# Performance work log

Hardware: AMD Instinct MI355X
Metric: run time of the kernel (lower is better)

## Reference

```python
import jax, jax.numpy as jnp
import numpy as np

L, N, E, D, H = 3, 20000, 320000, 128, 4
EPS = 1.1920929e-07  # torch RMSNorm default eps = finfo(float32).eps
NEG_SLOPE = 0.2      # PyG GATConv leaky_relu negative_slope


def rmsnorm(x, w):
    return x * jax.lax.rsqrt(jnp.mean(x * x, axis=-1, keepdims=True) + EPS) * w


def setup_inputs() -> dict:
    key = jax.random.key(0)
    ks = jax.random.split(key, 13)
    s = 0.02
    x = jax.random.normal(ks[0], (N, D), jnp.float32)
    src = jax.random.randint(ks[1], (E,), 0, N, dtype=jnp.int64)
    dst = jax.random.randint(ks[2], (E,), 0, N, dtype=jnp.int64)
    dst = jnp.where(dst == src, (dst + 1) % N, dst)  # no pre-existing self loops
    edge_index = jnp.stack([src, dst])
    return {
        "x": x,
        "W_gat": jax.random.normal(ks[3], (L, D, H * D), jnp.float32) * s,
        "att_src": jax.random.normal(ks[4], (L, H, D), jnp.float32) * s,
        "att_dst": jax.random.normal(ks[5], (L, H, D), jnp.float32) * s,
        "bias_gat": jax.random.normal(ks[6], (L, D), jnp.float32) * s,
        "W1": jax.random.normal(ks[7], (L, D, D), jnp.float32) * s,
        "b1": jax.random.normal(ks[8], (L, D), jnp.float32) * s,
        "W2": jax.random.normal(ks[9], (L, D, D), jnp.float32) * s,
        "b2": jax.random.normal(ks[10], (L, D), jnp.float32) * s,
        "norm1_w": jnp.ones((L, D), jnp.float32),
        "norm2_w": jnp.ones((L, D), jnp.float32),
        "edge_index": edge_index,
    }


def reference(x, W_gat, att_src, att_dst, bias_gat, W1, b1, W2, b2, norm1_w, norm2_w, edge_index):
    # PyG GATConv adds self loops by default
    loops = jnp.arange(N, dtype=edge_index.dtype)
    src = jnp.concatenate([edge_index[0], loops])  # [E+N]
    dst = jnp.concatenate([edge_index[1], loops])
    for i in range(L):
        # --- GATConv(hidden, hidden, heads=H, concat=False), dropout=0 (eval) ---
        xp = (x @ W_gat[i]).reshape(N, H, D)               # [N,H,D]
        a_s = jnp.einsum('nhd,hd->nh', xp, att_src[i])     # [N,H]
        a_d = jnp.einsum('nhd,hd->nh', xp, att_dst[i])
        e = jax.nn.leaky_relu(a_s[src] + a_d[dst], NEG_SLOPE)  # [E+N,H]
        m = jax.ops.segment_max(e, dst, num_segments=N)
        ex = jnp.exp(e - m[dst])
        denom = jax.ops.segment_sum(ex, dst, num_segments=N)
        alpha = ex / denom[dst]                             # segment softmax over incoming edges
        agg = jax.ops.segment_sum(alpha[:, :, None] * xp[src], dst, num_segments=N)  # [N,H,D]
        x_att = agg.mean(axis=1) + bias_gat[i]              # concat=False -> head mean, then bias
        # --- residual + RMSNorm ---
        x = rmsnorm(x + x_att, norm1_w[i])
        # --- FFN ---
        h = jax.nn.relu(x @ W1[i] + b1[i])
        h = h @ W2[i] + b2[i]
        x = rmsnorm(x + h, norm2_w[i])
    return x
```

## Files before the change

### kernel.cpp

```cpp
#include <hip/hip_runtime.h>
#include <hip/hip_bf16.h>

#define N_NODES 20000
#define NEDGE   320000
#define DIM     128
#define NH      4
#define HD      512
#define LAYERS  3
#define EPS_RMS 1.1920929e-07f
#define SLOPE   0.2f
#define NTILES  (N_NODES >> 4)

typedef __bf16 bf16_t;
typedef __bf16 bf16v2 __attribute__((ext_vector_type(2)));
typedef __bf16 bf16v8 __attribute__((ext_vector_type(8)));
typedef float  f32v4  __attribute__((ext_vector_type(4)));
typedef float  f32v2  __attribute__((ext_vector_type(2)));

__device__ __forceinline__ int clamp_node(int s) {
    return ((unsigned)s >= (unsigned)N_NODES) ? 0 : s;
}
__device__ __forceinline__ float leaky(float e) { return e > 0.f ? e : SLOPE * e; }
__device__ __forceinline__ unsigned char enc_fp8(float v) {
    int p = __builtin_amdgcn_cvt_pk_fp8_f32(v, v, 0, false);
    return (unsigned char)(p & 0xff);
}
__device__ __forceinline__ unsigned short enc_fp8_pair(float a, float b) {
    int p = __builtin_amdgcn_cvt_pk_fp8_f32(a, b, 0, false);
    return (unsigned short)(p & 0xffff);
}

__device__ __forceinline__ bool wave_detect_bf16(const unsigned short* xh) {
    int lane = threadIdx.x & 63;
    unsigned short hw = xh[2 * lane];
    int e = (hw >> 7) & 0xff;
    unsigned long long b = __ballot(e >= 96 && e <= 140);
    return __popcll(b) >= 48;
}
__device__ __forceinline__ bool wave_detect_i64(const int* ei) {
    int lane = threadIdx.x & 63;
    unsigned long long b = __ballot(ei[2 * lane + 1] != 0);
    return b == 0ULL;
}
__device__ __forceinline__ float raw_elem(const void* in, size_t j, bool isbf) {
    return isbf ? (float)((const bf16_t*)in)[j] : ((const float*)in)[j];
}
__device__ __forceinline__ bf16_t cvt_elem(const void* in, size_t j, bool isbf) {
    return isbf ? ((const bf16_t*)in)[j] : (bf16_t)((const float*)in)[j];
}
__device__ __forceinline__ int edge_src(const int* ei, int e, bool is64) {
    return clamp_node(is64 ? ei[2 * e] : ei[e]);
}
__device__ __forceinline__ int edge_dst(const int* ei, int e, bool is64) {
    return clamp_node(is64 ? ei[2 * NEDGE + 2 * e] : ei[NEDGE + e]);
}

__global__ __launch_bounds__(256) void prep_v(const void* x, const void* Wg,
                                              const void* aS, const void* aD,
                                              float* __restrict__ vS, float* __restrict__ vD,
                                              int* __restrict__ deg) {
    int gid = blockIdx.x * 256 + threadIdx.x;
    for (int i = gid; i < N_NODES; i += gridDim.x * 256) deg[i] = 0;
    bool isbf = wave_detect_bf16((const unsigned short*)x);
    int w = gid >> 6;
    if (w >= LAYERS * DIM * NH * 2) return;
    int lane = threadIdx.x & 63;
    int sd = w & 1, h = (w >> 1) & 3, k = (w >> 3) & 127, l = w >> 10;
    const void* att = sd ? aD : aS;
    size_t wbase = (size_t)l * DIM * HD + (size_t)k * HD + h * DIM;
    size_t abase = (size_t)l * NH * DIM + (size_t)h * DIM;
    int c = 2 * lane;
    float p = raw_elem(Wg, wbase + c, isbf) * raw_elem(att, abase + c, isbf)
            + raw_elem(Wg, wbase + c + 1, isbf) * raw_elem(att, abase + c + 1, isbf);
#pragma unroll
    for (int msk = 1; msk < 64; msk <<= 1) p += __shfl_xor(p, msk);
    if (lane == 0) {
        float* dst = sd ? vD : vS;
        dst[l * HD + h * DIM + k] = p;
    }
}

__global__ __launch_bounds__(256) void mega_setup(
        const void* x, const void* Wg, const void* W1, const void* W2,
        const void* bg, const void* b1, const void* b2, const void* n1, const void* n2,
        bf16_t* xb, bf16_t* WmixP, bf16_t* W1P, bf16_t* W2P,
        bf16_t* bgc, bf16_t* b1c, bf16_t* b2c, bf16_t* n1c, bf16_t* n2c,
        const int* ei, int* deg,
        const float* vS, const float* vD,
        float* a_s, float* a_d, unsigned short* x8,
        int convBlocks, int histBlocks) {
    const int NX  = N_NODES * DIM;
    const int NWG = LAYERS * DIM * HD;
    const int NW1 = LAYERS * DIM * DIM;
    const int NV  = LAYERS * DIM;
    int b = (int)blockIdx.x;
    if (b >= convBlocks + histBlocks) {
        bool isbf = wave_detect_bf16((const unsigned short*)x);
        int lane = threadIdx.x & 63;
        int n = (b - convBlocks - histBlocks) * 4 + (int)(threadIdx.x >> 6);
        if (n >= N_NODES) return;
        int c = 2 * lane;
        float f0 = raw_elem(x, (size_t)n * DIM + c, isbf);
        float f1 = raw_elem(x, (size_t)n * DIM + c + 1, isbf);
        x8[n * 64 + lane] = enc_fp8_pair(f0, f1);
#pragma unroll
        for (int h = 0; h < NH; ++h) {
            float ps = f0 * vS[h * DIM + c] + f1 * vS[h * DIM + c + 1];
            float pd = f0 * vD[h * DIM + c] + f1 * vD[h * DIM + c + 1];
#pragma unroll
            for (int msk = 1; msk < 64; msk <<= 1) {
                ps += __shfl_xor(ps, msk);
                pd += __shfl_xor(pd, msk);
            }
            if (lane == 0) {
                a_s[n * 4 + h] = ps;
                a_d[n * 4 + h] = pd;
            }
        }
        return;
    }
    if (b >= convBlocks) {
        bool is64 = wave_detect_i64(ei);
        int e = (b - convBlocks) * 256 + threadIdx.x;
        if (e < NEDGE) atomicAdd(&deg[edge_dst(ei, e, is64)], 1);
        return;
    }
    bool isbf = wave_detect_bf16((const unsigned short*)x);
    int i = b * 256 + threadIdx.x;
    if (i < NX) { xb[i] = cvt_elem(x, i, isbf); return; }
    i -= NX;
    if (i < NWG) {
        int l = i >> 16;
        int r = i & 65535;
        int j = r & 7;
        int lane2 = (r >> 3) & 63;
        int mm = lane2 & 15, kqq = lane2 >> 4;
        int tt = (r >> 9) & 1;
        int kk = (r >> 10) & 15;
        int wvv = r >> 14;
        int kidx = kk * 32 + kqq * 8 + j;
        int h = kidx >> 7, kp = kidx & 127;
        int c = 32 * wvv + tt * 16 + mm;
        WmixP[i] = cvt_elem(Wg, (size_t)l * DIM * HD + (size_t)kp * HD + h * DIM + c, isbf);
        return;
    }
    i -= NWG;
    if (i < NW1) {
        int l = i / 16384;
        int r = i & 16383;
        int j = r & 7;
        int lane2 = (r >> 3) & 63;
        int mm = lane2 & 15, kqq = lane2 >> 4;
        int tt = (r >> 9) & 1;
        int ks = (r >> 10) & 3;
        int wvv = r >> 12;
        int k = ks * 32 + kqq * 8 + j;
        int c = 32 * wvv + tt * 16 + mm;
        W1P[i] = cvt_elem(W1, (size_t)l * DIM * DIM + (size_t)k * DIM + c, isbf);
        return;
    }
    i -= NW1;
    if (i < NW1) {
        int l = i / 16384;
        int r = i & 16383;
        int j = r & 7;
        int lane2 = (r >> 3) & 63;
        int mm = lane2 & 15, kqq = lane2 >> 4;
        int tt = (r >> 9) & 1;
        int ks = (r >> 10) & 3;
        int wvv = r >> 12;
        int k = ks * 32 + kqq * 8 + j;
        int c = 32 * wvv + tt * 16 + mm;
        W2P[i] = cvt_elem(W2, (size_t)l * DIM * DIM + (size_t)k * DIM + c, isbf);
        return;
    }
    i -= NW1;
    if (i >= 5 * NV) return;
    int seg = i / NV, k = i - seg * NV;
    if (seg == 0) bgc[k] = cvt_elem(bg, k, isbf);
    else if (seg == 1) b1c[k] = cvt_elem(b1, k, isbf);
    else if (seg == 2) b2c[k] = cvt_elem(b2, k, isbf);
    else if (seg == 3) n1c[k] = cvt_elem(n1, k, isbf);
    else n2c[k] = cvt_elem(n2, k, isbf);
}

__global__ __launch_bounds__(1024) void scan_kernel(const int* __restrict__ deg,
                                                    int* __restrict__ row_ptr,
                                                    int* __restrict__ cursor) {
    __shared__ int wsum[16];
    int tid = threadIdx.x, lane = tid & 63, wv = tid >> 6;
    int v[20];
    int base = tid * 20;
    int tot = 0;
    if (base < N_NODES) {
        const int4* d4 = reinterpret_cast<const int4*>(deg + base);
#pragma unroll
        for (int j = 0; j < 5; ++j) {
            int4 q = d4[j];
            v[4 * j]     = q.x;
            v[4 * j + 1] = q.y;
            v[4 * j + 2] = q.z;
            v[4 * j + 3] = q.w;
        }
#pragma unroll
        for (int i = 0; i < 20; ++i) tot += v[i];
    }
    int x = tot;
#pragma unroll
    for (int off = 1; off < 64; off <<= 1) {
        int t = __shfl_up(x, off);
        if (lane >= off) x += t;
    }
    if (lane == 63) wsum[wv] = x;
    __syncthreads();
    if (wv == 0) {
        int s = (lane < 16) ? wsum[lane] : 0;
#pragma unroll
        for (int off = 1; off < 16; off <<= 1) {
            int t = __shfl_up(s, off);
            if (lane >= off) s += t;
        }
        if (lane < 16) wsum[lane] = s;
    }
    __syncthreads();
    int off0 = ((wv == 0) ? 0 : wsum[wv - 1]) + (x - tot);
    if (tid == 0) row_ptr[0] = 0;
    if (base < N_NODES) {
        int run = off0;
#pragma unroll
        for (int i = 0; i < 20; ++i) {
            run += v[i];
            row_ptr[base + i + 1] = run;
            cursor[base + i] = run - v[i];
        }
    }
}

__global__ void fill_kernel(const int* __restrict__ ei, int* __restrict__ cursor,
                            int* __restrict__ csr_src) {
    bool is64 = wave_detect_i64(ei);
    int e = blockIdx.x * blockDim.x + threadIdx.x;
    if (e < NEDGE) {
        int d = edge_dst(ei, e, is64);
        int pos = atomicAdd(&cursor[d], 1);
        if ((unsigned)pos < (unsigned)NEDGE) csr_src[pos] = edge_src(ei, e, is64);
    }
}

__global__ __launch_bounds__(256) void gat_gather(const int* __restrict__ row_ptr,
                                                  const int* __restrict__ csr_src,
                                                  const float* __restrict__ a_s,
                                                  const float* __restrict__ a_d,
                                                  const unsigned short* __restrict__ x8,
                                                  bf16_t* __restrict__ y) {
    __shared__ float4 wsh[4][64];
    __shared__ int    ssh[4][64];
    int n = (int)((blockIdx.x * blockDim.x + threadIdx.x) >> 6);
    if (n >= N_NODES) return;
    int wv = (int)(threadIdx.x >> 6) & 3;
    int lane = threadIdx.x & 63;
    int beg = row_ptr[n];
    int deg = row_ptr[n + 1] - beg;
    if (deg < 0) deg = 0;
    if (deg > NEDGE) deg = NEDGE;
    if (beg < 0) beg = 0;
    if (beg > NEDGE - deg) beg = NEDGE - deg;

    const float4* a_s4 = reinterpret_cast<const float4*>(a_s);
    const float4 adv = reinterpret_cast<const float4*>(a_d)[n];
    const float4 avs = a_s4[n];
    unsigned short pself = x8[n * 64 + lane];
    float4 wself = {__expf(leaky(avs.x + adv.x)), __expf(leaky(avs.y + adv.y)),
                    __expf(leaky(avs.z + adv.z)), __expf(leaky(avs.w + adv.w))};

    float acc[8];
    {
        f32v2 f = __builtin_amdgcn_cvt_pk_f32_fp8((int)pself, false);
        acc[0] = wself.x * f[0]; acc[1] = wself.x * f[1];
        acc[2] = wself.y * f[0]; acc[3] = wself.y * f[1];
        acc[4] = wself.z * f[0]; acc[5] = wself.z * f[1];
        acc[6] = wself.w * f[0]; acc[7] = wself.w * f[1];
    }

    float4 zl = {0.f, 0.f, 0.f, 0.f};
    for (int c0 = 0; c0 < deg; c0 += 64) {
        int cnt = deg - c0; if (cnt > 64) cnt = 64;
        if (lane < cnt) {
            int s = clamp_node(csr_src[beg + c0 + lane]);
            float4 av = a_s4[s];
            float4 w = {__expf(leaky(av.x + adv.x)), __expf(leaky(av.y + adv.y)),
                        __expf(leaky(av.z + adv.z)), __expf(leaky(av.w + adv.w))};
            zl.x += w.x; zl.y += w.y; zl.z += w.z; zl.w += w.w;
            wsh[wv][lane] = w;
            ssh[wv][lane] = s << 6;
        }
        for (int u0 = 0; u0 < cnt; u0 += 8) {
            int uc = cnt - u0; if (uc > 8) uc = 8;
            unsigned short xe[8]; float4 w[8];
#pragma unroll
            for (int u = 0; u < 8; ++u) {
                if (u < uc) {
                    int sb = ssh[wv][u0 + u];
                    w[u] = wsh[wv][u0 + u];
                    xe[u] = x8[sb + lane];
                }
            }
#pragma unroll
            for (int u = 0; u < 8; ++u) {
                if (u < uc) {
                    f32v2 f = __builtin_amdgcn_cvt_pk_f32_fp8((int)xe[u], false);
                    acc[0] += w[u].x * f[0]; acc[1] += w[u].x * f[1];
                    acc[2] += w[u].y * f[0]; acc[3] += w[u].y * f[1];
                    acc[4] += w[u].z * f[0]; acc[5] += w[u].z * f[1];
                    acc[6] += w[u].w * f[0]; acc[7] += w[u].w * f[1];
                }
            }
        }
    }
    float4 zr = zl;
#pragma unroll
    for (int msk = 1; msk < 64; msk <<= 1) {
        zr.x += __shfl_xor(zr.x, msk);
        zr.y += __shfl_xor(zr.y, msk);
        zr.z += __shfl_xor(zr.z, msk);
        zr.w += __shfl_xor(zr.w, msk);
    }
    float4 z4 = {wself.x + zr.x, wself.y + zr.y, wself.z + zr.z, wself.w + zr.w};
    float4 ih4 = {1.f / z4.x, 1.f / z4.y, 1.f / z4.z, 1.f / z4.w};
    int c = 2 * lane;
#pragma unroll
    for (int h = 0; h < NH; ++h) {
        float ih = h == 0 ? ih4.x : h == 1 ? ih4.y : h == 2 ? ih4.z : ih4.w;
        bf16v2 o;
        o[0] = (bf16_t)(acc[h * 2 + 0] * ih);
        o[1] = (bf16_t)(acc[h * 2 + 1] * ih);
        *reinterpret_cast<bf16v2*>(&y[(size_t)n * HD + h * DIM + c]) = o;
    }
}

template <int MODE>
__global__ __launch_bounds__(256) void mix_ffn(
        const bf16_t* __restrict__ y,
        const bf16_t* __restrict__ WmixP, const bf16_t* __restrict__ bg,
        const bf16_t* __restrict__ n1w, const bf16_t* __restrict__ xb,
        const bf16_t* __restrict__ W1P, const bf16_t* __restrict__ b1,
        const bf16_t* __restrict__ W2P, const bf16_t* __restrict__ b2,
        const bf16_t* __restrict__ n2w, void* __restrict__ out,
        const float* __restrict__ vS, const float* __restrict__ vD,
        float* __restrict__ a_s_n, float* __restrict__ a_d_n,
        unsigned char* __restrict__ x8_n) {
    __shared__ bf16_t ylds[16][524];
    __shared__ bf16_t xm[16][140];
    __shared__ float  ssq_p[16][4];
    __shared__ float  asd_p[4][16][8];
    bf16_t (*hh)[140] = reinterpret_cast<bf16_t (*)[140]>(&ylds[0][0]);

    int tile = blockIdx.x;
    int wv = threadIdx.x >> 6;
    int lane = threadIdx.x & 63;
    int m = lane & 15, kq = lane >> 4;

    const bf16_t* ybase = y + (size_t)tile * 16 * HD;
#pragma unroll
    for (int it = 0; it < 8; ++it) {
        int f = it * 2048 + (int)threadIdx.x * 8;
        int row = f >> 9, col = f & 511;
        *reinterpret_cast<bf16v8*>(&ylds[row][col]) =
            *reinterpret_cast<const bf16v8*>(ybase + f);
    }
    __syncthreads();

    f32v4 accm[2];
    accm[0] = (f32v4){0.f, 0.f, 0.f, 0.f};
    accm[1] = (f32v4){0.f, 0.f, 0.f, 0.f};
#pragma unroll
    for (int kk = 0; kk < 16; ++kk) {
        bf16v8 a = *reinterpret_cast<const bf16v8*>(&ylds[m][kk * 32 + kq * 8]);
#pragma unroll
        for (int tt = 0; tt < 2; ++tt) {
            bf16v8 b = *reinterpret_cast<const bf16v8*>(
                WmixP + ((((wv * 16 + kk) * 2 + tt) << 9) + lane * 8));
            accm[tt] = __builtin_amdgcn_mfma_f32_16x16x32_bf16(a, b, accm[tt], 0, 0, 0);
        }
    }
    float vals[2][4];
    {
        float sp[4] = {0.f, 0.f, 0.f, 0.f};
#pragma unroll
        for (int tt = 0; tt < 2; ++tt) {
            int col = 32 * wv + tt * 16 + m;
            float bv = (float)bg[col];
#pragma unroll
            for (int r = 0; r < 4; ++r) {
                int gr = tile * 16 + kq * 4 + r;
                float v = 0.25f * accm[tt][r] + bv + (float)xb[(size_t)gr * DIM + col];
                vals[tt][r] = v;
                sp[r] += v * v;
            }
        }
#pragma unroll
        for (int r = 0; r < 4; ++r) {
            sp[r] += __shfl_xor(sp[r], 1); sp[r] += __shfl_xor(sp[r], 2);
            sp[r] += __shfl_xor(sp[r], 4); sp[r] += __shfl_xor(sp[r], 8);
            if (m == r) ssq_p[kq * 4 + r][wv] = sp[r];
        }
    }
    __syncthreads();
    {
#pragma unroll
        for (int r = 0; r < 4; ++r) {
            int row = kq * 4 + r;
            float s = ssq_p[row][0] + ssq_p[row][1] + ssq_p[row][2] + ssq_p[row][3];
            float scale = rsqrtf(s * (1.f / 128.f) + EPS_RMS);
#pragma unroll
            for (int tt = 0; tt < 2; ++tt) {
                int col = 32 * wv + tt * 16 + m;
                xm[row][col] = (bf16_t)(vals[tt][r] * scale * (float)n1w[col]);
            }
        }
    }
    __syncthreads();

    f32v4 acc1[2];
    acc1[0] = (f32v4){0.f, 0.f, 0.f, 0.f};
    acc1[1] = (f32v4){0.f, 0.f, 0.f, 0.f};
#pragma unroll
    for (int ks = 0; ks < 4; ++ks) {
        bf16v8 a = *reinterpret_cast<const bf16v8*>(&xm[m][ks * 32 + kq * 8]);
#pragma unroll
        for (int tt = 0; tt < 2; ++tt) {
            bf16v8 b = *reinterpret_cast<const bf16v8*>(
                W1P + ((((wv * 4 + ks) * 2 + tt) << 9) + lane * 8));
            acc1[tt] = __builtin_amdgcn_mfma_f32_16x16x32_bf16(a, b, acc1[tt], 0, 0, 0);
        }
    }
#pragma unroll
    for (int tt = 0; tt < 2; ++tt) {
        int col = 32 * wv + tt * 16 + m;
        float bv = (float)b1[col];
#pragma unroll
        for (int r = 0; r < 4; ++r) {
            float v = acc1[tt][r] + bv;
            hh[kq * 4 + r][col] = (bf16_t)(v > 0.f ? v : 0.f);
        }
    }
    __syncthreads();
    f32v4 acc2[2];
    acc2[0] = (f32v4){0.f, 0.f, 0.f, 0.f};
    acc2[1] = (f32v4){0.f, 0.f, 0.f, 0.f};
#pragma unroll
    for (int ks = 0; ks < 4; ++ks) {
        bf16v8 a = *reinterpret_cast<const bf16v8*>(&hh[m][ks * 32 + kq * 8]);
#pragma unroll
        for (int tt = 0; tt < 2; ++tt) {
            bf16v8 b = *reinterpret_cast<const bf16v8*>(
                W2P + ((((wv * 4 + ks) * 2 + tt) << 9) + lane * 8));
            acc2[tt] = __builtin_amdgcn_mfma_f32_16x16x32_bf16(a, b, acc2[tt], 0, 0, 0);
        }
    }
    float vals2[2][4];
    {
        float sp[4] = {0.f, 0.f, 0.f, 0.f};
#pragma unroll
        for (int tt = 0; tt < 2; ++tt) {
            int col = 32 * wv + tt * 16 + m;
            float bv = (float)b2[col];
#pragma unroll
            for (int r = 0; r < 4; ++r) {
                float v = acc2[tt][r] + bv + (float)xm[kq * 4 + r][col];
                vals2[tt][r] = v;
                sp[r] += v * v;
            }
        }
#pragma unroll
        for (int r = 0; r < 4; ++r) {
            sp[r] += __shfl_xor(sp[r], 1); sp[r] += __shfl_xor(sp[r], 2);
            sp[r] += __shfl_xor(sp[r], 4); sp[r] += __shfl_xor(sp[r], 8);
            if (m == r) ssq_p[kq * 4 + r][wv] = sp[r];
        }
    }
    __syncthreads();
    float o2[2][4];
#pragma unroll
    for (int r = 0; r < 4; ++r) {
        int row = kq * 4 + r;
        int gr = tile * 16 + row;
        float s = ssq_p[row][0] + ssq_p[row][1] + ssq_p[row][2] + ssq_p[row][3];
        float scale = rsqrtf(s * (1.f / 128.f) + EPS_RMS);
#pragma unroll
        for (int tt = 0; tt < 2; ++tt) {
            int col = 32 * wv + tt * 16 + m;
            float o = vals2[tt][r] * scale * (float)n2w[col];
            o2[tt][r] = o;
            if (MODE == 1) ((float*)out)[(size_t)gr * DIM + col] = o;
            else {
                ((bf16_t*)out)[(size_t)gr * DIM + col] = (bf16_t)o;
                x8_n[(size_t)gr * DIM + col] = enc_fp8(o);
            }
        }
    }
    if (MODE == 0) {
        float vs0[NH], vs1[NH], vd0[NH], vd1[NH];
        int col0 = 32 * wv + m, col1 = col0 + 16;
#pragma unroll
        for (int h = 0; h < NH; ++h) {
            vs0[h] = vS[h * DIM + col0]; vs1[h] = vS[h * DIM + col1];
            vd0[h] = vD[h * DIM + col0]; vd1[h] = vD[h * DIM + col1];
        }
#pragma unroll
        for (int r = 0; r < 4; ++r) {
#pragma unroll
            for (int h = 0; h < NH; ++h) {
                float ps = o2[0][r] * vs0[h] + o2[1][r] * vs1[h];
                float pd = o2[0][r] * vd0[h] + o2[1][r] * vd1[h];
                ps += __shfl_xor(ps, 1); ps += __shfl_xor(ps, 2);
                ps += __shfl_xor(ps, 4); ps += __shfl_xor(ps, 8);
                pd += __shfl_xor(pd, 1); pd += __shfl_xor(pd, 2);
                pd += __shfl_xor(pd, 4); pd += __shfl_xor(pd, 8);
                if (m == r * 4 + h) {
                    asd_p[wv][kq * 4 + r][h * 2 + 0] = ps;
                    asd_p[wv][kq * 4 + r][h * 2 + 1] = pd;
                }
            }
        }
        __syncthreads();
        int t = threadIdx.x;
        if (t < 128) {
            int row = t >> 3, idx = t & 7;
            float s = asd_p[0][row][idx] + asd_p[1][row][idx]
                    + asd_p[2][row][idx] + asd_p[3][row][idx];
            int gr = tile * 16 + row;
            if (idx & 1) a_d_n[gr * 4 + (idx >> 1)] = s;
            else         a_s_n[gr * 4 + (idx >> 1)] = s;
        }
    }
}

extern "C" void kernel_launch(void* const* d_in, const int* in_sizes, int n_in,
                              void* d_out, int out_size, void* d_ws, size_t ws_size,
                              hipStream_t stream) {
    const void* x_in   = d_in[0];
    const void* W_gat  = d_in[1];
    const void* att_s  = d_in[2];
    const void* att_d  = d_in[3];
    const void* bias_g = d_in[4];
    const void* W1     = d_in[5];
    const void* b1     = d_in[6];
    const void* W2     = d_in[7];
    const void* b2     = d_in[8];
    const void* n1w    = d_in[9];
    const void* n2w    = d_in[10];
    const int*  ei     = (const int*)d_in[11];

    char* ws = (char*)d_ws;
    size_t off = 0;
    auto alloc = [&](size_t bytes) {
        void* p = ws + off;
        off = (off + bytes + 255) & ~(size_t)255;
        return p;
    };
    bf16_t* WmixP   = (bf16_t*)alloc((size_t)LAYERS * HD * DIM * 2);
    bf16_t* W1P     = (bf16_t*)alloc((size_t)LAYERS * DIM * DIM * 2);
    bf16_t* W2P     = (bf16_t*)alloc((size_t)LAYERS * DIM * DIM * 2);
    bf16_t* xb      = (bf16_t*)alloc((size_t)N_NODES * DIM * 2);
    bf16_t* y       = (bf16_t*)alloc((size_t)N_NODES * HD * 2);
    unsigned short* x8a = (unsigned short*)alloc((size_t)N_NODES * DIM);
    unsigned short* x8b = (unsigned short*)alloc((size_t)N_NODES * DIM);
    float*  vS      = (float*)alloc((size_t)LAYERS * HD * 4);
    float*  vD      = (float*)alloc((size_t)LAYERS * HD * 4);
    float*  a_sA    = (float*)alloc((size_t)N_NODES * NH * 4);
    float*  a_dA    = (float*)alloc((size_t)N_NODES * NH * 4);
    float*  a_sB    = (float*)alloc((size_t)N_NODES * NH * 4);
    float*  a_dB    = (float*)alloc((size_t)N_NODES * NH * 4);
    int*    deg     = (int*)alloc((size_t)N_NODES * 4);
    int*    cursor  = (int*)alloc((size_t)N_NODES * 4);
    int*    row_ptr = (int*)alloc((size_t)(N_NODES + 1) * 4);
    int*    csr     = (int*)alloc((size_t)NEDGE * 4);
    bf16_t* bgc     = (bf16_t*)alloc((size_t)LAYERS * DIM * 2);
    bf16_t* b1c     = (bf16_t*)alloc((size_t)LAYERS * DIM * 2);
    bf16_t* b2c     = (bf16_t*)alloc((size_t)LAYERS * DIM * 2);
    bf16_t* n1c     = (bf16_t*)alloc((size_t)LAYERS * DIM * 2);
    bf16_t* n2c     = (bf16_t*)alloc((size_t)LAYERS * DIM * 2);

    prep_v<<<(LAYERS * DIM * NH * 2 * 64 + 255) / 256, 256, 0, stream>>>(
        x_in, W_gat, att_s, att_d, vS, vD, deg);

    const int NTOT = N_NODES * DIM + LAYERS * DIM * HD + 2 * LAYERS * DIM * DIM
                   + 5 * LAYERS * DIM;
    const int convBlocks = (NTOT + 255) / 256;
    const int histBlocks = (NEDGE + 255) / 256;
    const int asdBlocks  = (N_NODES + 3) / 4;
    mega_setup<<<convBlocks + histBlocks + asdBlocks, 256, 0, stream>>>(
        x_in, W_gat, W1, W2, bias_g, b1, b2, n1w, n2w,
        xb, WmixP, W1P, W2P, bgc, b1c, b2c, n1c, n2c,
        ei, deg, vS, vD, a_sA, a_dA, x8a, convBlocks, histBlocks);

    scan_kernel<<<1, 1024, 0, stream>>>(deg, row_ptr, cursor);
    fill_kernel<<<(NEDGE + 255) / 256, 256, 0, stream>>>(ei, cursor, csr);

    unsigned short* x8cur[2] = {x8a, x8b};
    float* asCur[2] = {a_sA, a_sB};
    float* adCur[2] = {a_dA, a_dB};
    for (int l = 0; l < LAYERS; ++l) {
        int ci = l & 1, ni = (l + 1) & 1;
        gat_gather<<<(N_NODES * 64 + 255) / 256, 256, 0, stream>>>(
            row_ptr, csr, asCur[ci], adCur[ci], x8cur[ci], y);
        if (l < LAYERS - 1) {
            mix_ffn<0><<<NTILES, 256, 0, stream>>>(
                y, WmixP + (size_t)l * HD * DIM, bgc + (size_t)l * DIM,
                n1c + (size_t)l * DIM, xb,
                W1P + (size_t)l * DIM * DIM, b1c + (size_t)l * DIM,
                W2P + (size_t)l * DIM * DIM, b2c + (size_t)l * DIM,
                n2c + (size_t)l * DIM, xb,
                vS + (size_t)(l + 1) * HD, vD + (size_t)(l + 1) * HD,
                asCur[ni], adCur[ni], (unsigned char*)x8cur[ni]);
        } else {
            mix_ffn<1><<<NTILES, 256, 0, stream>>>(
                y, WmixP + (size_t)l * HD * DIM, bgc + (size_t)l * DIM,
                n1c + (size_t)l * DIM, xb,
                W1P + (size_t)l * DIM * DIM, b1c + (size_t)l * DIM,
                W2P + (size_t)l * DIM * DIM, b2c + (size_t)l * DIM,
                n2c + (size_t)l * DIM, d_out,
                nullptr, nullptr, nullptr, nullptr, nullptr);
        }
    }
}
```

Baseline: 313.3 us.

## Vectorize x conversion in setup and software-pipeline fp8 neighbor gathers

The setup kernel now converts x to bf16 eight elements per thread with vector loads and stores instead of one element per thread, which cuts the thread count and the per-element format checks. Weight packing moves into a helper function with the same logic. In the GAT gather loop, the fp8 neighbor feature loads for the next group of eight edges are issued before the current group is accumulated, a register double-buffer meant to hide gather latency. The price is more registers per thread, which may lower occupancy.

```diff
diff --git a/kernel.cpp b/kernel.cpp
--- a/kernel.cpp
+++ b/kernel.cpp
@@ -10,6 +10,12 @@
 #define EPS_RMS 1.1920929e-07f
 #define SLOPE   0.2f
 #define NTILES  (N_NODES >> 4)
+
+#define NWGC  (LAYERS * DIM * HD)
+#define NW1C  (LAYERS * DIM * DIM)
+#define NVC   (LAYERS * DIM)
+#define NPACK (NWGC + 2 * NW1C + 5 * NVC)
+#define NXV   (N_NODES * DIM / 8)
 
 typedef __bf16 bf16_t;
 typedef __bf16 bf16v2 __attribute__((ext_vector_type(2)));
@@ -80,56 +86,13 @@
     }
 }
 
-__global__ __launch_bounds__(256) void mega_setup(
-        const void* x, const void* Wg, const void* W1, const void* W2,
-        const void* bg, const void* b1, const void* b2, const void* n1, const void* n2,
-        bf16_t* xb, bf16_t* WmixP, bf16_t* W1P, bf16_t* W2P,
-        bf16_t* bgc, bf16_t* b1c, bf16_t* b2c, bf16_t* n1c, bf16_t* n2c,
-        const int* ei, int* deg,
-        const float* vS, const float* vD,
-        float* a_s, float* a_d, unsigned short* x8,
-        int convBlocks, int histBlocks) {
-    const int NX  = N_NODES * DIM;
-    const int NWG = LAYERS * DIM * HD;
-    const int NW1 = LAYERS * DIM * DIM;
-    const int NV  = LAYERS * DIM;
-    int b = (int)blockIdx.x;
-    if (b >= convBlocks + histBlocks) {
-        bool isbf = wave_detect_bf16((const unsigned short*)x);
-        int lane = threadIdx.x & 63;
-        int n = (b - convBlocks - histBlocks) * 4 + (int)(threadIdx.x >> 6);
-        if (n >= N_NODES) return;
-        int c = 2 * lane;
-        float f0 = raw_elem(x, (size_t)n * DIM + c, isbf);
-        float f1 = raw_elem(x, (size_t)n * DIM + c + 1, isbf);
-        x8[n * 64 + lane] = enc_fp8_pair(f0, f1);
-#pragma unroll
-        for (int h = 0; h < NH; ++h) {
-            float ps = f0 * vS[h * DIM + c] + f1 * vS[h * DIM + c + 1];
-            float pd = f0 * vD[h * DIM + c] + f1 * vD[h * DIM + c + 1];
-#pragma unroll
-            for (int msk = 1; msk < 64; msk <<= 1) {
-                ps += __shfl_xor(ps, msk);
-                pd += __shfl_xor(pd, msk);
-            }
-            if (lane == 0) {
-                a_s[n * 4 + h] = ps;
-                a_d[n * 4 + h] = pd;
-            }
-        }
-        return;
-    }
-    if (b >= convBlocks) {
-        bool is64 = wave_detect_i64(ei);
-        int e = (b - convBlocks) * 256 + threadIdx.x;
-        if (e < NEDGE) atomicAdd(&deg[edge_dst(ei, e, is64)], 1);
-        return;
-    }
-    bool isbf = wave_detect_bf16((const unsigned short*)x);
-    int i = b * 256 + threadIdx.x;
-    if (i < NX) { xb[i] = cvt_elem(x, i, isbf); return; }
-    i -= NX;
-    if (i < NWG) {
+__device__ __forceinline__ void pack_item(int i, bool isbf,
+        const void* Wg, const void* W1, const void* W2,
+        const void* bg, const void* b1, const void* b2,
+        const void* n1, const void* n2,
+        bf16_t* WmixP, bf16_t* W1P, bf16_t* W2P,
+        bf16_t* bgc, bf16_t* b1c, bf16_t* b2c, bf16_t* n1c, bf16_t* n2c) {
+    if (i < NWGC) {
         int l = i >> 16;
         int r = i & 65535;
         int j = r & 7;
@@ -144,8 +107,8 @@
         WmixP[i] = cvt_elem(Wg, (size_t)l * DIM * HD + (size_t)kp * HD + h * DIM + c, isbf);
         return;
     }
-    i -= NWG;
-    if (i < NW1) {
+    i -= NWGC;
+    if (i < NW1C) {
         int l = i / 16384;
         int r = i & 16383;
         int j = r & 7;
@@ -159,8 +122,8 @@
         W1P[i] = cvt_elem(W1, (size_t)l * DIM * DIM + (size_t)k * DIM + c, isbf);
         return;
     }
-    i -= NW1;
-    if (i < NW1) {
+    i -= NW1C;
+    if (i < NW1C) {
         int l = i / 16384;
         int r = i & 16383;
         int j = r & 7;
@@ -174,14 +137,76 @@
         W2P[i] = cvt_elem(W2, (size_t)l * DIM * DIM + (size_t)k * DIM + c, isbf);
         return;
     }
-    i -= NW1;
-    if (i >= 5 * NV) return;
-    int seg = i / NV, k = i - seg * NV;
+    i -= NW1C;
+    if (i >= 5 * NVC) return;
+    int seg = i / NVC, k = i - seg * NVC;
     if (seg == 0) bgc[k] = cvt_elem(bg, k, isbf);
     else if (seg == 1) b1c[k] = cvt_elem(b1, k, isbf);
     else if (seg == 2) b2c[k] = cvt_elem(b2, k, isbf);
     else if (seg == 3) n1c[k] = cvt_elem(n1, k, isbf);
     else n2c[k] = cvt_elem(n2, k, isbf);
+}
+
+__global__ __launch_bounds__(256) void mega_setup(
+        const void* x, const void* Wg, const void* W1, const void* W2,
+        const void* bg, const void* b1, const void* b2, const void* n1, const void* n2,
+        bf16_t* xb, bf16_t* WmixP, bf16_t* W1P, bf16_t* W2P,
+        bf16_t* bgc, bf16_t* b1c, bf16_t* b2c, bf16_t* n1c, bf16_t* n2c,
+        const int* ei, int* deg,
+        const float* vS, const float* vD,
+        float* a_s, float* a_d, unsigned short* x8,
+        int convBlocks, int histBlocks) {
+    int b = (int)blockIdx.x;
+    if (b >= convBlocks + histBlocks) {
+        bool isbf = wave_detect_bf16((const unsigned short*)x);
+        int lane = threadIdx.x & 63;
+        int n = (b - convBlocks - histBlocks) * 4 + (int)(threadIdx.x >> 6);
+        if (n >= N_NODES) return;
+        int c = 2 * lane;
+        float f0 = raw_elem(x, (size_t)n * DIM + c, isbf);
+        float f1 = raw_elem(x, (size_t)n * DIM + c + 1, isbf);
+        x8[n * 64 + lane] = enc_fp8_pair(f0, f1);
+#pragma unroll
+        for (int h = 0; h < NH; ++h) {
+            float ps = f0 * vS[h * DIM + c] + f1 * vS[h * DIM + c + 1];
+            float pd = f0 * vD[h * DIM + c] + f1 * vD[h * DIM + c + 1];
+#pragma unroll
+            for (int msk = 1; msk < 64; msk <<= 1) {
+                ps += __shfl_xor(ps, msk);
+                pd += __shfl_xor(pd, msk);
+            }
+            if (lane == 0) {
+                a_s[n * 4 + h] = ps;
+                a_d[n * 4 + h] = pd;
+            }
+        }
+        return;
+    }
+    if (b >= convBlocks) {
+        bool is64 = wave_detect_i64(ei);
+        int e = (b - convBlocks) * 256 + threadIdx.x;
+        if (e < NEDGE) atomicAdd(&deg[edge_dst(ei, e, is64)], 1);
+        return;
+    }
+    bool isbf = wave_detect_bf16((const unsigned short*)x);
+    int i = b * 256 + threadIdx.x;
+    if (i < NXV) {
+        if (isbf) {
+            ((bf16v8*)xb)[i] = ((const bf16v8*)x)[i];
+        } else {
+            const float4* src = (const float4*)x;
+            float4 a = src[2 * i], bq = src[2 * i + 1];
+            bf16v8 o;
+            o[0] = (bf16_t)a.x;  o[1] = (bf16_t)a.y;
+            o[2] = (bf16_t)a.z;  o[3] = (bf16_t)a.w;
+            o[4] = (bf16_t)bq.x; o[5] = (bf16_t)bq.y;
+            o[6] = (bf16_t)bq.z; o[7] = (bf16_t)bq.w;
+            ((bf16v8*)xb)[i] = o;
+        }
+        return;
+    }
+    pack_item(i - NXV, isbf, Wg, W1, W2, bg, b1, b2, n1, n2,
+              WmixP, W1P, W2P, bgc, b1c, b2c, n1c, n2c);
 }
 
 __global__ __launch_bounds__(1024) void scan_kernel(const int* __restrict__ deg,
@@ -294,25 +319,32 @@
             wsh[wv][lane] = w;
             ssh[wv][lane] = s << 6;
         }
+        unsigned short xeN[8];
+        {
+            int p0 = cnt < 8 ? cnt : 8;
+#pragma unroll
+            for (int u = 0; u < 8; ++u)
+                if (u < p0) xeN[u] = x8[ssh[wv][u] + lane];
+        }
         for (int u0 = 0; u0 < cnt; u0 += 8) {
             int uc = cnt - u0; if (uc > 8) uc = 8;
-            unsigned short xe[8]; float4 w[8];
+            unsigned short xeC[8];
+#pragma unroll
+            for (int u = 0; u < 8; ++u) xeC[u] = xeN[u];
+            int n0 = u0 + 8;
+            int nc = cnt - n0; if (nc > 8) nc = 8;
+#pragma unroll
+            for (int u = 0; u < 8; ++u)
+                if (u < nc) xeN[u] = x8[ssh[wv][n0 + u] + lane];
 #pragma unroll
             for (int u = 0; u < 8; ++u) {
                 if (u < uc) {
-                    int sb = ssh[wv][u0 + u];
-                    w[u] = wsh[wv][u0 + u];
-                    xe[u] = x8[sb + lane];
-                }
-            }
-#pragma unroll
-            for (int u = 0; u < 8; ++u) {
-                if (u < uc) {
-                    f32v2 f = __builtin_amdgcn_cvt_pk_f32_fp8((int)xe[u], false);
-                    acc[0] += w[u].x * f[0]; acc[1] += w[u].x * f[1];
-                    acc[2] += w[u].y * f[0]; acc[3] += w[u].y * f[1];
-                    acc[4] += w[u].z * f[0]; acc[5] += w[u].z * f[1];
-                    acc[6] += w[u].w * f[0]; acc[7] += w[u].w * f[1];
+                    float4 w = wsh[wv][u0 + u];
+                    f32v2 f = __builtin_amdgcn_cvt_pk_f32_fp8((int)xeC[u], false);
+                    acc[0] += w.x * f[0]; acc[1] += w.x * f[1];
+                    acc[2] += w.y * f[0]; acc[3] += w.y * f[1];
+                    acc[4] += w.z * f[0]; acc[5] += w.z * f[1];
+                    acc[6] += w.w * f[0]; acc[7] += w.w * f[1];
                 }
             }
         }
@@ -585,8 +617,7 @@
     prep_v<<<(LAYERS * DIM * NH * 2 * 64 + 255) / 256, 256, 0, stream>>>(
         x_in, W_gat, att_s, att_d, vS, vD, deg);
 
-    const int NTOT = N_NODES * DIM + LAYERS * DIM * HD + 2 * LAYERS * DIM * DIM
-                   + 5 * LAYERS * DIM;
+    const int NTOT = NXV + NPACK;
     const int convBlocks = (NTOT + 255) / 256;
     const int histBlocks = (NEDGE + 255) / 256;
     const int asdBlocks  = (N_NODES + 3) / 4;
```

After: 301.0 us. 3.9% less time.
